# Kernel tuning notes

Hardware: AMD Instinct MI355X
Metric: run time of the kernel (lower is better)

Reference implementation:

```python
import jax, jax.numpy as jnp
import numpy as np

EMBED_DIM = 1024
NUM_HEADS = 16
HEAD_DIM = EMBED_DIM // NUM_HEADS
BATCH = 2
SEQ = 2048


def setup_inputs() -> dict:
    key = jax.random.key(0)
    ks = jax.random.split(key, 9)
    s = 1.0 / np.sqrt(EMBED_DIM)
    return {
        "x": jax.random.normal(ks[0], (BATCH, SEQ, EMBED_DIM), jnp.float32),
        "mask": jnp.ones((BATCH, SEQ), jnp.int32),
        "Wq": jax.random.normal(ks[1], (EMBED_DIM, EMBED_DIM), jnp.float32) * s,
        "bq": jax.random.normal(ks[2], (EMBED_DIM,), jnp.float32) * s,
        "Wk": jax.random.normal(ks[3], (EMBED_DIM, EMBED_DIM), jnp.float32) * s,
        "bk": jax.random.normal(ks[4], (EMBED_DIM,), jnp.float32) * s,
        "Wv": jax.random.normal(ks[5], (EMBED_DIM, EMBED_DIM), jnp.float32) * s,
        "bv": jax.random.normal(ks[6], (EMBED_DIM,), jnp.float32) * s,
        "Wo": jax.random.normal(ks[7], (EMBED_DIM, EMBED_DIM), jnp.float32) * s,
        "bo": jax.random.normal(ks[8], (EMBED_DIM,), jnp.float32) * s,
    }


def reference(x, mask, Wq, bq, Wk, bk, Wv, bv, Wo, bo):
    B, S, E = x.shape
    H, D = NUM_HEADS, HEAD_DIM
    # torch Linear: y = x @ W.T + b
    q = (x @ Wq.T + bq).reshape(B, S, H, D).transpose(0, 2, 1, 3)  # [B,H,S,D]
    k = (x @ Wk.T + bk).reshape(B, S, H, D).transpose(0, 2, 1, 3)
    v = (x @ Wv.T + bv).reshape(B, S, H, D).transpose(0, 2, 1, 3)
    scores = jnp.einsum("bhqd,bhkd->bhqk", q, k) / jnp.sqrt(jnp.float32(D))
    # mask: [B,S] -> [B,1,1,S]; fill masked positions with -1e9
    scores = jnp.where(mask[:, None, None, :] == 0, jnp.float32(-1e9), scores)
    probs = jax.nn.softmax(scores, axis=-1)
    # dropout omitted: original stores a float and would crash; eval semantics = identity
    attn = jnp.einsum("bhqk,bhkd->bhqd", probs, v)  # [B,H,S,D]
    attn = attn.transpose(0, 2, 1, 3).reshape(B, S, E)
    return attn @ Wo.T + bo
```

## Files before the change

kernel.cpp:

```cpp
#include <hip/hip_runtime.h>
#include <stdint.h>

#define S_LEN 2048
#define EMB   1024
#define NH    16
#define HD    64
#define BK 64

typedef __bf16 bf16x8 __attribute__((ext_vector_type(8)));
typedef short  short4v __attribute__((ext_vector_type(4)));
typedef unsigned int uint2v __attribute__((ext_vector_type(2)));
typedef unsigned int uint4v __attribute__((ext_vector_type(4)));
typedef float  floatx4 __attribute__((ext_vector_type(4)));

#if defined(__has_builtin)
#if __has_builtin(__builtin_amdgcn_mfma_f32_16x16x16bf16_1k)
#define HAVE_MFMA16 1
#endif
#if __has_builtin(__builtin_amdgcn_exp2f)
#define EXP2F __builtin_amdgcn_exp2f
#endif
#endif
#ifndef EXP2F
#define EXP2F exp2f
#endif

#define QSCALE 0.1803368801111204f

__device__ __forceinline__ unsigned short f2bf(float f) {
  unsigned u = __builtin_bit_cast(unsigned, f);
  u += 0x7fffu + ((u >> 16) & 1u);
  return (unsigned short)(u >> 16);
}
__device__ __forceinline__ unsigned short f2bf_hu(float f) {
  return (unsigned short)((__builtin_bit_cast(unsigned, f) + 0x8000u) >> 16);
}
__device__ __forceinline__ unsigned packbf2(float a, float b) {
  unsigned ua = __builtin_bit_cast(unsigned, a) + 0x8000u;
  unsigned ub = __builtin_bit_cast(unsigned, b) + 0x8000u;
  return __builtin_amdgcn_perm(ub, ua, 0x07060302);
}

__global__ __launch_bounds__(256) void cvt_all(const float* __restrict__ x,
                                               const float* __restrict__ Wq,
                                               const float* __restrict__ Wk,
                                               const float* __restrict__ Wv,
                                               const float* __restrict__ Wo,
                                               unsigned short* __restrict__ xb,
                                               unsigned short* __restrict__ Wqb,
                                               unsigned short* __restrict__ Wkb,
                                               unsigned short* __restrict__ Wvb,
                                               unsigned short* __restrict__ Wob) {
  int blk = blockIdx.x;
  const float* s; unsigned short* d; int off;
  if (blk < 4096)      { s = x;  d = xb;  off = blk; }
  else if (blk < 5120) { s = Wq; d = Wqb; off = blk - 4096; }
  else if (blk < 6144) { s = Wk; d = Wkb; off = blk - 5120; }
  else if (blk < 7168) { s = Wv; d = Wvb; off = blk - 6144; }
  else                 { s = Wo; d = Wob; off = blk - 7168; }
  int i = (off * 256 + threadIdx.x) * 4;
  float4 v = *(const float4*)(s + i);
  ushort4 o;
  o.x = f2bf(v.x); o.y = f2bf(v.y); o.z = f2bf(v.z); o.w = f2bf(v.w);
  *(ushort4*)(d + i) = o;
}

__device__ __forceinline__ void stage16(const void* g, void* l) {
  __builtin_amdgcn_global_load_lds(
      (const __attribute__((address_space(1))) void*)g,
      (__attribute__((address_space(3))) void*)l, 16, 0, 0);
}

__global__ __launch_bounds__(256, 3) void qkv_gemm(const unsigned short* __restrict__ xb,
                                                   const unsigned short* __restrict__ Wqb,
                                                   const unsigned short* __restrict__ Wkb,
                                                   const unsigned short* __restrict__ Wvb,
                                                   const float* __restrict__ bq,
                                                   const float* __restrict__ bk,
                                                   const float* __restrict__ bv,
                                                   unsigned short* __restrict__ Qb,
                                                   unsigned short* __restrict__ Kb,
                                                   unsigned short* __restrict__ Vtb) {
  __shared__ unsigned short Sh[2 * 128 * BK];
  unsigned short* As = Sh;
  unsigned short* Bs = Sh + 128 * BK;

  const int lid = blockIdx.x + 32 * blockIdx.y + 256 * blockIdx.z;
  const int xcd = lid & 7;
  const int seq = lid >> 3;
  const int z   = seq >> 5;
  const int ml  = (seq & 31) >> 3;
  const int nb  = seq & 7;
  const int m0 = (xcd * 4 + ml) * 128;
  const int n0 = nb * 128;

  const unsigned short* Bm = (z == 0) ? Wqb : (z == 1) ? Wkb : Wvb;
  const float* bias        = (z == 0) ? bq  : (z == 1) ? bk  : bv;
  unsigned short* outp     = (z == 0) ? Qb  : (z == 1) ? Kb  : Vtb;
  const float scale = (z == 0) ? QSCALE : 1.0f;
  const int mode = (z == 2) ? 2 : 1;

  const int tid  = threadIdx.x;
  const int lane = tid & 63;
  const int wave = tid >> 6;
  const int m16  = lane & 15;
  const int quad = lane >> 4;
  const int wrow = (wave >> 1) * 64;
  const int wcol = (wave & 1) * 64;
  const int K = 1024;

  floatx4 acc[4][4];
  for (int i = 0; i < 4; ++i)
    for (int j = 0; j < 4; ++j) acc[i][j] = floatx4{0.f, 0.f, 0.f, 0.f};

  for (int k0 = 0; k0 < K; k0 += BK) {
    __syncthreads();
    for (int i = 0; i < 4; ++i) {
      int c = i * 256 + tid;
      int row = c >> 3, col = (c & 7) << 3;
      stage16(xb + (size_t)(m0 + row) * K + k0 + col,
              (char*)As + (size_t)(i * 256 + wave * 64) * 16);
      stage16(Bm + (size_t)(n0 + row) * K + k0 + col,
              (char*)Bs + (size_t)(i * 256 + wave * 64) * 16);
    }
    __syncthreads();
    for (int kk = 0; kk < 2; ++kk) {
      bf16x8 af[4], bfr[4];
      for (int ti = 0; ti < 4; ++ti)
        af[ti] = *(const bf16x8*)(As + (wrow + ti * 16 + m16) * BK + kk * 32 + quad * 8);
      for (int tj = 0; tj < 4; ++tj)
        bfr[tj] = *(const bf16x8*)(Bs + (wcol + tj * 16 + m16) * BK + kk * 32 + quad * 8);
      for (int ti = 0; ti < 4; ++ti)
        for (int tj = 0; tj < 4; ++tj)
          acc[ti][tj] = __builtin_amdgcn_mfma_f32_16x16x32_bf16(bfr[tj], af[ti], acc[ti][tj], 0, 0, 0);
    }
  }

  __syncthreads();
  const int bb = m0 >> 11, ss0 = m0 & 2047;

  if (mode == 1) {
    for (int ti = 0; ti < 4; ++ti) {
      int m = wrow + ti * 16 + m16;
      for (int tj = 0; tj < 4; ++tj) {
        int col = wcol + tj * 16 + quad * 4;
        int c8 = col >> 3, off = col & 7;
        float4 b4 = *(const float4*)(bias + n0 + col);
        float v0 = (acc[ti][tj][0] + b4.x) * scale;
        float v1 = (acc[ti][tj][1] + b4.y) * scale;
        float v2 = (acc[ti][tj][2] + b4.z) * scale;
        float v3 = (acc[ti][tj][3] + b4.w) * scale;
        unsigned* cw = (unsigned*)&Sh[m * 128 + ((c8 ^ (m & 7)) << 3) + off];
        cw[0] = packbf2(v0, v1);
        cw[1] = packbf2(v2, v3);
      }
    }
    __syncthreads();
    for (int e = 0; e < 8; ++e) {
      int g = e * 256 + tid;
      int hf = g >> 10;
      int gg = g & 1023;
      int m = gg >> 3, c8l = gg & 7;
      uint4v v = *(const uint4v*)&Sh[m * 128 + (((hf * 8 + c8l) ^ (m & 7)) << 3)];
      int hh = (n0 >> 6) + hf;
      unsigned short* dst = outp + ((size_t)(bb * NH + hh) * S_LEN + ss0 + m) * HD + c8l * 8;
      *(uint4v*)dst = v;
    }
  } else {
    for (int tj = 0; tj < 4; ++tj)
      for (int reg = 0; reg < 4; ++reg) {
        int n = wcol + tj * 16 + quad * 4 + reg;
        float bv = bias[n0 + n];
        for (int ti = 0; ti < 4; ++ti) {
          int m = wrow + ti * 16 + m16;
          int cm = m >> 3;
          Sh[n * 128 + ((cm ^ (n & 15)) << 3) + (m & 7)] =
              f2bf_hu(acc[ti][tj][reg] + bv);
        }
      }
    __syncthreads();
    for (int e = 0; e < 8; ++e) {
      int g = e * 256 + tid;
      int n = g >> 4, cm = g & 15;
      uint4v v = *(const uint4v*)&Sh[n * 128 + ((cm ^ (n & 15)) << 3)];
      int gn = n0 + n, hh = gn >> 6, d = gn & 63;
      unsigned short* dst = outp + ((size_t)(bb * NH + hh) * HD + d) * S_LEN + ss0 + cm * 8;
      *(uint4v*)dst = v;
    }
  }
}

__global__ __launch_bounds__(256, 4) void out_gemm(const unsigned short* __restrict__ Ab,
                                                   const unsigned short* __restrict__ Wob,
                                                   const float* __restrict__ bo,
                                                   float* __restrict__ out) {
  __shared__ unsigned short As[128 * BK];
  __shared__ unsigned short Bs[64 * BK];
  const int lid = blockIdx.x + 32 * blockIdx.y;
  const int xcd = lid & 7;
  const int seq = lid >> 3;
  const int m0 = (xcd * 4 + (seq >> 4)) * 128;
  const int n0 = (seq & 15) * 64;

  const int tid  = threadIdx.x;
  const int lane = tid & 63;
  const int wave = tid >> 6;
  const int m16  = lane & 15;
  const int quad = lane >> 4;
  const int wrow = (wave >> 1) * 64;
  const int wcol = (wave & 1) * 32;
  const int K = 1024, N = 1024;

  floatx4 acc[4][2];
  for (int i = 0; i < 4; ++i)
    for (int j = 0; j < 2; ++j) acc[i][j] = floatx4{0.f, 0.f, 0.f, 0.f};

  for (int k0 = 0; k0 < K; k0 += BK) {
    __syncthreads();
    for (int i = 0; i < 4; ++i) {
      int c = i * 256 + tid;
      int row = c >> 3, col = (c & 7) << 3;
      stage16(Ab + (size_t)(m0 + row) * K + k0 + col,
              (char*)As + (size_t)(i * 256 + wave * 64) * 16);
    }
    for (int i = 0; i < 2; ++i) {
      int c = i * 256 + tid;
      int row = c >> 3, col = (c & 7) << 3;
      stage16(Wob + (size_t)(n0 + row) * K + k0 + col,
              (char*)Bs + (size_t)(i * 256 + wave * 64) * 16);
    }
    __syncthreads();
    for (int kk = 0; kk < 2; ++kk) {
      bf16x8 af[4], bfr[2];
      for (int ti = 0; ti < 4; ++ti)
        af[ti] = *(const bf16x8*)(As + (wrow + ti * 16 + m16) * BK + kk * 32 + quad * 8);
      for (int tj = 0; tj < 2; ++tj)
        bfr[tj] = *(const bf16x8*)(Bs + (wcol + tj * 16 + m16) * BK + kk * 32 + quad * 8);
      for (int ti = 0; ti < 4; ++ti)
        for (int tj = 0; tj < 2; ++tj)
          acc[ti][tj] = __builtin_amdgcn_mfma_f32_16x16x32_bf16(af[ti], bfr[tj], acc[ti][tj], 0, 0, 0);
    }
  }

  for (int tj = 0; tj < 2; ++tj) {
    int n = n0 + wcol + tj * 16 + m16;
    float bv = bo[n];
    for (int ti = 0; ti < 4; ++ti)
      for (int reg = 0; reg < 4; ++reg) {
        int m = m0 + wrow + ti * 16 + quad * 4 + reg;
        out[(size_t)m * N + n] = acc[ti][tj][reg] + bv;
      }
  }
}

__global__ __launch_bounds__(256, 4) void attn_kernel(const unsigned short* __restrict__ Qb,
                                                      const unsigned short* __restrict__ Kb,
                                                      const unsigned short* __restrict__ Vtb,
                                                      const int* __restrict__ mask,
                                                      unsigned short* __restrict__ attnb) {
  __shared__ unsigned short Ks[2 * 64 * 64];
  __shared__ unsigned short Vts[2 * 64 * 64];
  __shared__ int zw[4];
#ifndef HAVE_MFMA16
  __shared__ unsigned short Pq[4 * 16 * 72];
#endif

  const int tid  = threadIdx.x;
  const int lane = tid & 63;
  const int wave = tid >> 6;
  const int m16  = lane & 15;
  const int quad = lane >> 4;
  const int bh = blockIdx.x;
  const int qt = blockIdx.y;
  const int b  = bh >> 4;
  const int h  = bh & 15;
  const int q0 = qt * 128;
  const size_t head = (size_t)bh * S_LEN * HD;

  bf16x8 qf[2][2];
  for (int qs = 0; qs < 2; ++qs) {
    const unsigned short* qrow = Qb + head + (size_t)(q0 + wave * 32 + qs * 16 + m16) * HD;
    qf[qs][0] = *(const bf16x8*)(qrow + quad * 8);
    qf[qs][1] = *(const bf16x8*)(qrow + 32 + quad * 8);
  }

  const int kr = lane >> 3, kc = lane & 7;
  const unsigned short* kg0 = Kb + head + (size_t)(wave * 16 + kr) * HD + ((kc ^ kr) << 3);
  const unsigned short* vg0 = Vtb + head + (size_t)(wave * 16 + kr) * S_LEN + ((kc ^ kr) << 3);
  const int* mrow = mask + b * S_LEN;

#define STAGE_KV(pp, kb_)                                                      \
  {                                                                            \
    const unsigned short* ksrc = kg0 + (size_t)(kb_) * 64 * HD;                \
    char* kdst = (char*)Ks + (pp) * 8192 + wave * 2048;                        \
    stage16(ksrc,           kdst);                                             \
    stage16(ksrc + 8 * HD,  kdst + 1024);                                      \
    const unsigned short* vsrc = vg0 + (kb_) * 64;                             \
    char* vdst = (char*)Vts + (pp) * 8192 + wave * 2048;                       \
    stage16(vsrc,              vdst);                                          \
    stage16(vsrc + 8 * S_LEN,  vdst + 1024);                                   \
  }

  float l_run[2] = {0.f, 0.f};
  floatx4 acc_o[2][4];
  for (int qs = 0; qs < 2; ++qs)
    for (int ti = 0; ti < 4; ++ti) acc_o[qs][ti] = floatx4{0.f, 0.f, 0.f, 0.f};

  {
    const int4* mp = (const int4*)(mrow + tid * 8);
    int4 a = mp[0], c4 = mp[1];
    bool z = (a.x & a.y & a.z & a.w & c4.x & c4.y & c4.z & c4.w) == 0;
    unsigned long long bal = __ballot(z);
    if (lane == 0) zw[wave] = (bal != 0ull) ? 1 : 0;
  }

  STAGE_KV(0, 0);
  __syncthreads();
  const bool anymask = (zw[0] | zw[1] | zw[2] | zw[3]) != 0;

  const int xs = m16 & 7;
  const floatx4 fz = floatx4{0.f, 0.f, 0.f, 0.f};

  for (int kb = 0; kb < 32; ++kb) {
    const int p = kb & 1;
    const unsigned short* Kp = Ks + p * 4096;
    const unsigned short* Vp = Vts + p * 4096;
    if (kb < 31) STAGE_KV(p ^ 1, kb + 1);

    floatx4 acc_s[2][4];
    {
      bf16x8 kf[4];
      for (int tj = 0; tj < 4; ++tj)
        kf[tj] = *(const bf16x8*)&Kp[(tj * 16 + m16) * 64 + ((quad ^ xs) << 3)];
      for (int tj = 0; tj < 4; ++tj) {
        acc_s[0][tj] = __builtin_amdgcn_mfma_f32_16x16x32_bf16(kf[tj], qf[0][0], fz, 0, 0, 0);
        acc_s[1][tj] = __builtin_amdgcn_mfma_f32_16x16x32_bf16(kf[tj], qf[1][0], fz, 0, 0, 0);
      }
      for (int tj = 0; tj < 4; ++tj)
        kf[tj] = *(const bf16x8*)&Kp[(tj * 16 + m16) * 64 + (((4 + quad) ^ xs) << 3)];
      for (int tj = 0; tj < 4; ++tj) {
        acc_s[0][tj] = __builtin_amdgcn_mfma_f32_16x16x32_bf16(kf[tj], qf[0][1], acc_s[0][tj], 0, 0, 0);
        acc_s[1][tj] = __builtin_amdgcn_mfma_f32_16x16x32_bf16(kf[tj], qf[1][1], acc_s[1][tj], 0, 0, 0);
      }
    }

    unsigned up[2][8];
    for (int qs = 0; qs < 2; ++qs) {
      if (anymask) {
        for (int t = 0; t < 4; ++t)
          for (int r = 0; r < 4; ++r) {
            int idx = kb * 64 + t * 16 + quad * 4 + r;
            acc_s[qs][t][r] += (mrow[idx] == 0) ? -1e9f : 0.f;
          }
      }
      float sl = 0.f;
      for (int i = 0; i < 8; ++i) {
        float p0 = EXP2F(acc_s[qs][i >> 1][(i & 1) * 2]);
        float p1 = EXP2F(acc_s[qs][i >> 1][(i & 1) * 2 + 1]);
        sl += p0 + p1;
        up[qs][i] = packbf2(p0, p1);
      }
      l_run[qs] += sl;
    }

#ifdef HAVE_MFMA16
    for (int ti = 0; ti < 4; ++ti)
      for (int c = 0; c < 4; ++c) {
        short4v vf = *(const short4v*)&Vp[(ti * 16 + m16) * 64 +
                                          (((2 * c + (quad >> 1)) ^ xs) << 3) +
                                          ((quad & 1) << 2)];
        short4v Pb0 = __builtin_bit_cast(short4v, uint2v{up[0][2 * c], up[0][2 * c + 1]});
        short4v Pb1 = __builtin_bit_cast(short4v, uint2v{up[1][2 * c], up[1][2 * c + 1]});
        acc_o[0][ti] = __builtin_amdgcn_mfma_f32_16x16x16bf16_1k(vf, Pb0, acc_o[0][ti], 0, 0, 0);
        acc_o[1][ti] = __builtin_amdgcn_mfma_f32_16x16x16bf16_1k(vf, Pb1, acc_o[1][ti], 0, 0, 0);
      }
#else
    {
      unsigned short* Pw = Pq + wave * 16 * 72;
      for (int qs = 0; qs < 2; ++qs) {
        for (int t = 0; t < 4; ++t) {
          *(unsigned*)&Pw[m16 * 72 + t * 16 + quad * 4]     = up[qs][2 * t];
          *(unsigned*)&Pw[m16 * 72 + t * 16 + quad * 4 + 2] = up[qs][2 * t + 1];
        }
        for (int kk = 0; kk < 2; ++kk) {
          bf16x8 pf = *(const bf16x8*)&Pw[m16 * 72 + kk * 32 + quad * 8];
          for (int ti = 0; ti < 4; ++ti) {
            bf16x8 vfb = *(const bf16x8*)&Vp[(ti * 16 + m16) * 64 +
                                             (((kk * 4 + quad) ^ xs) << 3)];
            acc_o[qs][ti] = __builtin_amdgcn_mfma_f32_16x16x32_bf16(vfb, pf, acc_o[qs][ti], 0, 0, 0);
          }
        }
      }
    }
#endif

    __syncthreads();
  }

  for (int qs = 0; qs < 2; ++qs) {
    l_run[qs] += __shfl_xor(l_run[qs], 16);
    l_run[qs] += __shfl_xor(l_run[qs], 32);
    float rl = 1.f / l_run[qs];
    int orow = q0 + wave * 32 + qs * 16 + m16;
    for (int ti = 0; ti < 4; ++ti) {
      ushort4 o;
      o.x = f2bf_hu(acc_o[qs][ti][0] * rl);
      o.y = f2bf_hu(acc_o[qs][ti][1] * rl);
      o.z = f2bf_hu(acc_o[qs][ti][2] * rl);
      o.w = f2bf_hu(acc_o[qs][ti][3] * rl);
      int e = h * HD + ti * 16 + quad * 4;
      *(ushort4*)&attnb[((size_t)(b * S_LEN + orow)) * EMB + e] = o;
    }
  }
#undef STAGE_KV
}

extern "C" void kernel_launch(void* const* d_in, const int* in_sizes, int n_in,
                              void* d_out, int out_size, void* d_ws, size_t ws_size,
                              hipStream_t stream) {
  const float* x  = (const float*)d_in[0];
  const int* mask = (const int*)d_in[1];
  const float* Wq = (const float*)d_in[2];
  const float* bq = (const float*)d_in[3];
  const float* Wk = (const float*)d_in[4];
  const float* bk = (const float*)d_in[5];
  const float* Wv = (const float*)d_in[6];
  const float* bv = (const float*)d_in[7];
  const float* Wo = (const float*)d_in[8];
  const float* bo = (const float*)d_in[9];
  float* out = (float*)d_out;

  char* ws = (char*)d_ws;
  unsigned short* xb  = (unsigned short*)(ws);
  unsigned short* Ab  = (unsigned short*)(ws);
  unsigned short* Wqb = (unsigned short*)(ws + 8388608);
  unsigned short* Wkb = (unsigned short*)(ws + 10485760);
  unsigned short* Wvb = (unsigned short*)(ws + 12582912);
  unsigned short* Wob = (unsigned short*)(ws + 14680064);
  unsigned short* Qb  = (unsigned short*)(ws + 16777216);
  unsigned short* Kbb = (unsigned short*)(ws + 25165824);
  unsigned short* Vtb = (unsigned short*)(ws + 33554432);

  cvt_all<<<dim3(8192), dim3(256), 0, stream>>>(x, Wq, Wk, Wv, Wo, xb, Wqb, Wkb, Wvb, Wob);
  qkv_gemm<<<dim3(32, 8, 3), dim3(256), 0, stream>>>(xb, Wqb, Wkb, Wvb, bq, bk, bv, Qb, Kbb, Vtb);
  attn_kernel<<<dim3(32, 16), dim3(256), 0, stream>>>(Qb, Kbb, Vtb, mask, Ab);
  out_gemm<<<dim3(32, 16), dim3(256), 0, stream>>>(Ab, Wob, bo, out);
}
```

Measured before the change: 200.1 us.

## Software-pipeline attention loop with triple-buffered KV and QK lookahead

Restructures the attention inner loop so the QK^T MFMAs for the next key block run before the softmax and PV of the current block, letting matrix and exp work interleave. K/V staging moves from double to triple buffering so the prefetch runs two blocks ahead. s_setprio is raised around the MFMA sections. Launch bounds drop from 4 to 2 blocks per SM to leave room for the extra registers and shared memory, at the cost of lower occupancy.

```diff
diff --git a/kernel.cpp b/kernel.cpp
--- a/kernel.cpp
+++ b/kernel.cpp
@@ -23,6 +23,15 @@
 #endif
 #ifndef EXP2F
 #define EXP2F exp2f
+#endif
+
+#if defined(__has_builtin)
+#if __has_builtin(__builtin_amdgcn_s_setprio)
+#define SETPRIO(x) __builtin_amdgcn_s_setprio(x)
+#endif
+#endif
+#ifndef SETPRIO
+#define SETPRIO(x)
 #endif
 
 #define QSCALE 0.1803368801111204f
@@ -253,13 +262,13 @@
   }
 }
 
-__global__ __launch_bounds__(256, 4) void attn_kernel(const unsigned short* __restrict__ Qb,
+__global__ __launch_bounds__(256, 2) void attn_kernel(const unsigned short* __restrict__ Qb,
                                                       const unsigned short* __restrict__ Kb,
                                                       const unsigned short* __restrict__ Vtb,
                                                       const int* __restrict__ mask,
                                                       unsigned short* __restrict__ attnb) {
-  __shared__ unsigned short Ks[2 * 64 * 64];
-  __shared__ unsigned short Vts[2 * 64 * 64];
+  __shared__ unsigned short Ks[3 * 64 * 64];
+  __shared__ unsigned short Vts[3 * 64 * 64];
   __shared__ int zw[4];
 #ifndef HAVE_MFMA16
   __shared__ unsigned short Pq[4 * 16 * 72];
@@ -314,56 +323,51 @@
     if (lane == 0) zw[wave] = (bal != 0ull) ? 1 : 0;
   }
 
-  STAGE_KV(0, 0);
-  __syncthreads();
-  const bool anymask = (zw[0] | zw[1] | zw[2] | zw[3]) != 0;
-
   const int xs = m16 & 7;
   const floatx4 fz = floatx4{0.f, 0.f, 0.f, 0.f};
 
-  for (int kb = 0; kb < 32; ++kb) {
-    const int p = kb & 1;
-    const unsigned short* Kp = Ks + p * 4096;
-    const unsigned short* Vp = Vts + p * 4096;
-    if (kb < 31) STAGE_KV(p ^ 1, kb + 1);
-
-    floatx4 acc_s[2][4];
-    {
-      bf16x8 kf[4];
-      for (int tj = 0; tj < 4; ++tj)
-        kf[tj] = *(const bf16x8*)&Kp[(tj * 16 + m16) * 64 + ((quad ^ xs) << 3)];
-      for (int tj = 0; tj < 4; ++tj) {
-        acc_s[0][tj] = __builtin_amdgcn_mfma_f32_16x16x32_bf16(kf[tj], qf[0][0], fz, 0, 0, 0);
-        acc_s[1][tj] = __builtin_amdgcn_mfma_f32_16x16x32_bf16(kf[tj], qf[1][0], fz, 0, 0, 0);
-      }
-      for (int tj = 0; tj < 4; ++tj)
-        kf[tj] = *(const bf16x8*)&Kp[(tj * 16 + m16) * 64 + (((4 + quad) ^ xs) << 3)];
-      for (int tj = 0; tj < 4; ++tj) {
-        acc_s[0][tj] = __builtin_amdgcn_mfma_f32_16x16x32_bf16(kf[tj], qf[0][1], acc_s[0][tj], 0, 0, 0);
-        acc_s[1][tj] = __builtin_amdgcn_mfma_f32_16x16x32_bf16(kf[tj], qf[1][1], acc_s[1][tj], 0, 0, 0);
-      }
-    }
-
-    unsigned up[2][8];
+  auto qk_tile = [&](floatx4 (&as)[2][4], const unsigned short* Kp) {
+    bf16x8 kf[4];
+    SETPRIO(1);
+    for (int tj = 0; tj < 4; ++tj)
+      kf[tj] = *(const bf16x8*)&Kp[(tj * 16 + m16) * 64 + ((quad ^ xs) << 3)];
+    for (int tj = 0; tj < 4; ++tj) {
+      as[0][tj] = __builtin_amdgcn_mfma_f32_16x16x32_bf16(kf[tj], qf[0][0], fz, 0, 0, 0);
+      as[1][tj] = __builtin_amdgcn_mfma_f32_16x16x32_bf16(kf[tj], qf[1][0], fz, 0, 0, 0);
+    }
+    for (int tj = 0; tj < 4; ++tj)
+      kf[tj] = *(const bf16x8*)&Kp[(tj * 16 + m16) * 64 + (((4 + quad) ^ xs) << 3)];
+    for (int tj = 0; tj < 4; ++tj) {
+      as[0][tj] = __builtin_amdgcn_mfma_f32_16x16x32_bf16(kf[tj], qf[0][1], as[0][tj], 0, 0, 0);
+      as[1][tj] = __builtin_amdgcn_mfma_f32_16x16x32_bf16(kf[tj], qf[1][1], as[1][tj], 0, 0, 0);
+    }
+    SETPRIO(0);
+  };
+
+  auto softmax_tile = [&](floatx4 (&as)[2][4], int kb, unsigned (&up)[2][8]) {
+    const bool am = (zw[0] | zw[1] | zw[2] | zw[3]) != 0;
     for (int qs = 0; qs < 2; ++qs) {
-      if (anymask) {
+      if (am) {
         for (int t = 0; t < 4; ++t)
           for (int r = 0; r < 4; ++r) {
             int idx = kb * 64 + t * 16 + quad * 4 + r;
-            acc_s[qs][t][r] += (mrow[idx] == 0) ? -1e9f : 0.f;
+            as[qs][t][r] += (mrow[idx] == 0) ? -1e9f : 0.f;
           }
       }
       float sl = 0.f;
       for (int i = 0; i < 8; ++i) {
-        float p0 = EXP2F(acc_s[qs][i >> 1][(i & 1) * 2]);
-        float p1 = EXP2F(acc_s[qs][i >> 1][(i & 1) * 2 + 1]);
+        float p0 = EXP2F(as[qs][i >> 1][(i & 1) * 2]);
+        float p1 = EXP2F(as[qs][i >> 1][(i & 1) * 2 + 1]);
         sl += p0 + p1;
         up[qs][i] = packbf2(p0, p1);
       }
       l_run[qs] += sl;
     }
-
+  };
+
+  auto pv_tile = [&](unsigned (&up)[2][8], const unsigned short* Vp) {
 #ifdef HAVE_MFMA16
+    SETPRIO(1);
     for (int ti = 0; ti < 4; ++ti)
       for (int c = 0; c < 4; ++c) {
         short4v vf = *(const short4v*)&Vp[(ti * 16 + m16) * 64 +
@@ -374,27 +378,54 @@
         acc_o[0][ti] = __builtin_amdgcn_mfma_f32_16x16x16bf16_1k(vf, Pb0, acc_o[0][ti], 0, 0, 0);
         acc_o[1][ti] = __builtin_amdgcn_mfma_f32_16x16x16bf16_1k(vf, Pb1, acc_o[1][ti], 0, 0, 0);
       }
+    SETPRIO(0);
 #else
+    unsigned short* Pw = Pq + wave * 16 * 72;
+    for (int qs = 0; qs < 2; ++qs) {
+      for (int t = 0; t < 4; ++t) {
+        *(unsigned*)&Pw[m16 * 72 + t * 16 + quad * 4]     = up[qs][2 * t];
+        *(unsigned*)&Pw[m16 * 72 + t * 16 + quad * 4 + 2] = up[qs][2 * t + 1];
+      }
+      for (int kk = 0; kk < 2; ++kk) {
+        bf16x8 pf = *(const bf16x8*)&Pw[m16 * 72 + kk * 32 + quad * 8];
+        for (int ti = 0; ti < 4; ++ti) {
+          bf16x8 vfb = *(const bf16x8*)&Vp[(ti * 16 + m16) * 64 +
+                                           (((kk * 4 + quad) ^ xs) << 3)];
+          acc_o[qs][ti] = __builtin_amdgcn_mfma_f32_16x16x32_bf16(vfb, pf, acc_o[qs][ti], 0, 0, 0);
+        }
+      }
+    }
+#endif
+  };
+
+  STAGE_KV(0, 0);
+  STAGE_KV(1, 1);
+  __syncthreads();
+
+  floatx4 accA[2][4], accB[2][4];
+  unsigned upA[2][8], upB[2][8];
+  qk_tile(accA, Ks + 0 * 4096);
+
+  int scur = 0, snxt = 1, sstg = 2;
+  for (int it = 0; it < 16; ++it) {
     {
-      unsigned short* Pw = Pq + wave * 16 * 72;
-      for (int qs = 0; qs < 2; ++qs) {
-        for (int t = 0; t < 4; ++t) {
-          *(unsigned*)&Pw[m16 * 72 + t * 16 + quad * 4]     = up[qs][2 * t];
-          *(unsigned*)&Pw[m16 * 72 + t * 16 + quad * 4 + 2] = up[qs][2 * t + 1];
-        }
-        for (int kk = 0; kk < 2; ++kk) {
-          bf16x8 pf = *(const bf16x8*)&Pw[m16 * 72 + kk * 32 + quad * 8];
-          for (int ti = 0; ti < 4; ++ti) {
-            bf16x8 vfb = *(const bf16x8*)&Vp[(ti * 16 + m16) * 64 +
-                                             (((kk * 4 + quad) ^ xs) << 3)];
-            acc_o[qs][ti] = __builtin_amdgcn_mfma_f32_16x16x32_bf16(vfb, pf, acc_o[qs][ti], 0, 0, 0);
-          }
-        }
-      }
-    }
-#endif
-
-    __syncthreads();
+      const int kbE = it * 2;
+      if (it < 15) STAGE_KV(sstg, kbE + 2);
+      qk_tile(accB, Ks + snxt * 4096);
+      softmax_tile(accA, kbE, upA);
+      pv_tile(upA, Vts + scur * 4096);
+      __syncthreads();
+      int t = scur; scur = snxt; snxt = sstg; sstg = t;
+    }
+    {
+      const int kbO = it * 2 + 1;
+      if (it < 15) STAGE_KV(sstg, kbO + 2);
+      if (it < 15) qk_tile(accA, Ks + snxt * 4096);
+      softmax_tile(accB, kbO, upB);
+      pv_tile(upB, Vts + scur * 4096);
+      __syncthreads();
+      int t = scur; scur = snxt; snxt = sstg; sstg = t;
+    }
   }
 
   for (int qs = 0; qs < 2; ++qs) {
```

Result: no change. 198.7 us (-0.7%).

## Triple-buffer K/V tiles in attention with manual vmcnt waits and raw barriers

Applied to the files above, without the earlier changes.

Switches the attention kernel's K/V shared-memory staging from double to triple buffering, prefetching two tiles ahead. The full __syncthreads is replaced with explicit s_waitcnt vmcnt counts plus s_barrier so that only the oldest stage has to land before the barrier. The goal is to hide global load latency behind the MFMA work. In exchange, shared memory grows by half and the launch_bounds occupancy hint drops from 4 to 2. Correctness now depends on STAGE_KV issuing exactly the number of vector memory ops that the hard-coded vmcnt(8) assumes.

```diff
diff --git a/kernel.cpp b/kernel.cpp
--- a/kernel.cpp
+++ b/kernel.cpp
@@ -20,9 +20,23 @@
 #if __has_builtin(__builtin_amdgcn_exp2f)
 #define EXP2F __builtin_amdgcn_exp2f
 #endif
+#if __has_builtin(__builtin_amdgcn_s_barrier)
+#define BAR() __builtin_amdgcn_s_barrier()
+#endif
 #endif
 #ifndef EXP2F
 #define EXP2F exp2f
+#endif
+#ifndef BAR
+#define BAR() __syncthreads()
+#endif
+
+#if defined(__HIP_DEVICE_COMPILE__)
+#define VMCNT(n)      asm volatile("s_waitcnt vmcnt(" #n ")" ::: "memory")
+#define VMCNT_LGKM(n) asm volatile("s_waitcnt vmcnt(" #n ") lgkmcnt(0)" ::: "memory")
+#else
+#define VMCNT(n)
+#define VMCNT_LGKM(n)
 #endif
 
 #define QSCALE 0.1803368801111204f
@@ -253,13 +267,13 @@
   }
 }
 
-__global__ __launch_bounds__(256, 4) void attn_kernel(const unsigned short* __restrict__ Qb,
+__global__ __launch_bounds__(256, 2) void attn_kernel(const unsigned short* __restrict__ Qb,
                                                       const unsigned short* __restrict__ Kb,
                                                       const unsigned short* __restrict__ Vtb,
                                                       const int* __restrict__ mask,
                                                       unsigned short* __restrict__ attnb) {
-  __shared__ unsigned short Ks[2 * 64 * 64];
-  __shared__ unsigned short Vts[2 * 64 * 64];
+  __shared__ unsigned short Ks[3 * 64 * 64];
+  __shared__ unsigned short Vts[3 * 64 * 64];
   __shared__ int zw[4];
 #ifndef HAVE_MFMA16
   __shared__ unsigned short Pq[4 * 16 * 72];
@@ -315,17 +329,19 @@
   }
 
   STAGE_KV(0, 0);
-  __syncthreads();
+  STAGE_KV(1, 1);
+  VMCNT_LGKM(8);
+  BAR();
   const bool anymask = (zw[0] | zw[1] | zw[2] | zw[3]) != 0;
 
   const int xs = m16 & 7;
   const floatx4 fz = floatx4{0.f, 0.f, 0.f, 0.f};
 
   for (int kb = 0; kb < 32; ++kb) {
-    const int p = kb & 1;
-    const unsigned short* Kp = Ks + p * 4096;
-    const unsigned short* Vp = Vts + p * 4096;
-    if (kb < 31) STAGE_KV(p ^ 1, kb + 1);
+    const int sl = kb % 3;
+    const unsigned short* Kp = Ks + sl * 4096;
+    const unsigned short* Vp = Vts + sl * 4096;
+    if (kb < 30) STAGE_KV((kb + 2) % 3, kb + 2);
 
     floatx4 acc_s[2][4];
     {
@@ -353,14 +369,14 @@
             acc_s[qs][t][r] += (mrow[idx] == 0) ? -1e9f : 0.f;
           }
       }
-      float sl = 0.f;
+      float sl2 = 0.f;
       for (int i = 0; i < 8; ++i) {
         float p0 = EXP2F(acc_s[qs][i >> 1][(i & 1) * 2]);
         float p1 = EXP2F(acc_s[qs][i >> 1][(i & 1) * 2 + 1]);
-        sl += p0 + p1;
+        sl2 += p0 + p1;
         up[qs][i] = packbf2(p0, p1);
       }
-      l_run[qs] += sl;
+      l_run[qs] += sl2;
     }
 
 #ifdef HAVE_MFMA16
@@ -394,7 +410,8 @@
     }
 #endif
 
-    __syncthreads();
+    if (kb < 30) { VMCNT(8); } else { VMCNT(0); }
+    BAR();
   }
 
   for (int qs = 0; qs < 2; ++qs) {
```

After: 200.2 us. About the same (+0.1%).
